# Performance work log

Hardware: AMD Instinct MI355X
Metric: run time of the kernel (lower is better)

## Reference

```python
import jax, jax.numpy as jnp
import numpy as np

V, E, H, O = 25000, 300, 512, 1
B, T = 128, 512


def setup_inputs() -> dict:
    key = jax.random.key(0)
    ks = jax.random.split(key, 8)
    # xavier-uniform style init for weight matrices
    def xav(k, shape):
        fan_in, fan_out = shape[1], shape[0]
        lim = jnp.sqrt(6.0 / (fan_in + fan_out)).astype(jnp.float32)
        return jax.random.uniform(k, shape, jnp.float32, -lim, lim)
    x = jax.random.randint(ks[0], (B, T), 0, V)
    h0 = jnp.zeros((1, B, H), jnp.float32)
    c0 = jnp.zeros((1, B, H), jnp.float32)
    emb = jax.random.normal(ks[1], (V, E), jnp.float32)
    W_ih = xav(ks[2], (4 * H, E))
    W_hh = xav(ks[3], (4 * H, H))
    b_ih = jnp.zeros((4 * H,), jnp.float32)
    b_hh = jnp.zeros((4 * H,), jnp.float32)
    fc_w = xav(ks[4], (O, H))
    fc_b = jnp.zeros((O,), jnp.float32)
    return {"x": x, "h0": h0, "c0": c0, "emb": emb, "W_ih": W_ih,
            "W_hh": W_hh, "b_ih": b_ih, "b_hh": b_hh, "fc_w": fc_w, "fc_b": fc_b}


def reference(x, h0, c0, emb, W_ih, W_hh, b_ih, b_hh, fc_w, fc_b):
    # embedding lookup: [B, T, E]
    embed = emb[x]
    # precompute input projections for all timesteps: [T, B, 4H]
    gates_x = jnp.einsum('bte,ge->tbg', embed, W_ih) + b_ih + b_hh

    def step(carry, gx):
        h, c = carry  # [B, H], [B, H]
        gates = gx + h @ W_hh.T  # [B, 4H]
        i, f, g, o = jnp.split(gates, 4, axis=-1)
        i = jax.nn.sigmoid(i)
        f = jax.nn.sigmoid(f)
        g = jnp.tanh(g)
        o = jax.nn.sigmoid(o)
        c = f * c + i * g
        h = o * jnp.tanh(c)
        return (h, c), h

    (h_T, c_T), hs = jax.lax.scan(step, (h0[0], c0[0]), gates_x)
    output = jnp.transpose(hs, (1, 0, 2))[None]  # [1, B, T, H]
    h_out = output[:, :, -1:]                     # [1, B, 1, H]
    c_out = c_T[None]                             # [1, B, H]
    y = h_out @ fc_w.T + fc_b                     # [1, B, 1, O]
    return y, h_out, c_out
```

## Files before the change

kernel.cpp:

```cpp
#include <hip/hip_runtime.h>

#define VOCAB 25000
#define EDIM  300
#define EPAD  320
#define HDIM  512
#define BATCH 128
#define TLEN  512
#define NTHR  512

typedef __attribute__((ext_vector_type(8))) short short8;
typedef __attribute__((ext_vector_type(4))) float f32x4;
typedef unsigned int u32;
typedef unsigned long long u64;

static __device__ __forceinline__ unsigned short f2bf(float f) {
    unsigned int u = __float_as_uint(f);
    unsigned int r = u + 0x7fffu + ((u >> 16) & 1u);
    return (unsigned short)(r >> 16);
}

__global__ void conv_pad_row(const float* __restrict__ src, unsigned short* __restrict__ dst,
                             int rows, int cs, int cd) {
    for (int r = blockIdx.x; r < rows; r += gridDim.x)
        for (int c = threadIdx.x; c < cd; c += blockDim.x)
            dst[(long)r * cd + c] = (c < cs) ? f2bf(src[(long)r * cs + c]) : (unsigned short)0;
}

__global__ __launch_bounds__(NTHR, 2) void lstm_pers(
    const int* __restrict__ x, const float* __restrict__ h0, const float* __restrict__ c0,
    const float* __restrict__ b_ih, const float* __restrict__ b_hh,
    const unsigned short* __restrict__ embb, const unsigned short* __restrict__ wihb,
    const unsigned short* __restrict__ whhb, u32* __restrict__ hb, float* __restrict__ out) {
    const int tid  = threadIdx.x;
    const int bt   = blockIdx.x & 7;
    const int jt   = blockIdx.x >> 3;
    const int m0   = bt * 16;
    const int lane = tid & 63;
    const int wv   = tid >> 6;
    const int gate = wv >> 1, jsub = wv & 1;
    const int g0   = gate * HDIM + jt * 32 + jsub * 16;
    const int r    = lane & 15;
    const int q    = lane >> 4;
    const int sw   = r & 7;

    const int bl = tid >> 5, jl = tid & 31;
    const int bg = m0 + bl, jg = jt * 32 + jl;

    __shared__ alignas(16) unsigned short h_lds[16 * 512];
    __shared__ alignas(16) unsigned short emb_lds[2][16 * 320];
    __shared__ int x_lds[16 * TLEN];
    __shared__ float lds_g[4][16][36];

    const int brow = g0 + r;
    const unsigned short* whp = whhb + (long)brow * HDIM + q * 8;
    const unsigned short* wip = wihb + (long)brow * EPAD + q * 8;
#define LDH(i) short8 wh##i = *(const short8*)(whp + i * 32);
#define LDE(i) short8 wi##i = *(const short8*)(wip + i * 32);
    LDH(0) LDH(1) LDH(2) LDH(3) LDH(4) LDH(5) LDH(6) LDH(7)
    LDH(8) LDH(9) LDH(10) LDH(11) LDH(12) LDH(13) LDH(14) LDH(15)
    LDE(0) LDE(1) LDE(2) LDE(3) LDE(4) LDE(5) LDE(6) LDE(7) LDE(8) LDE(9)
#undef LDH
#undef LDE

    for (int i = tid; i < 16 * TLEN; i += NTHR)
        x_lds[i] = x[(m0 + (i >> 9)) * TLEN + (i & 511)];

    const float bsum0 = b_ih[0 * HDIM + jg] + b_hh[0 * HDIM + jg];
    const float bsum1 = b_ih[1 * HDIM + jg] + b_hh[1 * HDIM + jg];
    const float bsum2 = b_ih[2 * HDIM + jg] + b_hh[2 * HDIM + jg];
    const float bsum3 = b_ih[3 * HDIM + jg] + b_hh[3 * HDIM + jg];

    float c_reg = c0[bg * HDIM + jg];
    float h_reg = h0[bg * HDIM + jg];

    u32* const hb0 = hb;
    u32* const hb1 = hb + BATCH * HDIM;
    __hip_atomic_store(hb0 + bg * HDIM + jg, (u32)f2bf(h_reg),
                       __ATOMIC_RELAXED, __HIP_MEMORY_SCOPE_AGENT);

    u32 hoff[8], lofs[8];
#pragma unroll
    for (int k = 0; k < 8; ++k) {
        int u   = tid + k * NTHR;
        int row = u >> 8, col = u & 255;
        hoff[k] = (u32)((m0 + row) * 256 + col);
        int chunk = col >> 2, sub = col & 3;
        lofs[k] = (u32)(row * 512 + ((chunk ^ (row & 7)) * 4 + sub) * 2);
    }

    __syncthreads();
    {
        int row = tid / 40, cc = tid - row * 40;
        int tok = x_lds[row * TLEN];
        *(short8*)&emb_lds[0][row * 320 + ((cc ^ (row & 7)) * 8)] =
            *(const short8*)(embb + (long)tok * EPAD + cc * 8);
        if (tid < 128) {
            int i1 = tid + NTHR; int row2 = i1 / 40, cc2 = i1 - row2 * 40;
            int tok2 = x_lds[row2 * TLEN];
            *(short8*)&emb_lds[0][row2 * 320 + ((cc2 ^ (row2 & 7)) * 8)] =
                *(const short8*)(embb + (long)tok2 * EPAD + cc2 * 8);
        }
    }
    __syncthreads();

    for (int t = 0; t < TLEN; ++t) {
        const int pb = t & 1;
        const u64* hsrc = (const u64*)(pb ? hb1 : hb0);
        u64 hv[8];
#pragma unroll
        for (int k = 0; k < 8; ++k)
            hv[k] = __hip_atomic_load(hsrc + hoff[k], __ATOMIC_RELAXED, __HIP_MEMORY_SCOPE_AGENT);

        {
            int tn = (t + 1 < TLEN) ? (t + 1) : (TLEN - 1);
            unsigned short* ebuf = (unsigned short*)emb_lds[pb ^ 1];
            int row = tid / 40, cc = tid - row * 40;
            int tok = x_lds[row * TLEN + tn];
            *(short8*)&ebuf[row * 320 + ((cc ^ (row & 7)) * 8)] =
                *(const short8*)(embb + (long)tok * EPAD + cc * 8);
            if (tid < 128) {
                int i1 = tid + NTHR; int row2 = i1 / 40, cc2 = i1 - row2 * 40;
                int tok2 = x_lds[row2 * TLEN + tn];
                *(short8*)&ebuf[row2 * 320 + ((cc2 ^ (row2 & 7)) * 8)] =
                    *(const short8*)(embb + (long)tok2 * EPAD + cc2 * 8);
            }
        }

        const unsigned short* ecur = (const unsigned short*)emb_lds[pb];
        f32x4 ae = {0.f, 0.f, 0.f, 0.f};
        short8 a;
#define ME(i) a = *(const short8*)&ecur[r * 320 + (((q + 4 * i) ^ sw) * 8)]; \
              ae = __builtin_amdgcn_mfma_f32_16x16x32_bf16(a, wi##i, ae, 0, 0, 0);
        ME(0) ME(1) ME(2) ME(3) ME(4) ME(5) ME(6) ME(7) ME(8) ME(9)
#undef ME

        const u32 want = (u32)t;
        while (1) {
            u32 bad = 0;
#pragma unroll
            for (int k = 0; k < 8; ++k)
                bad |= (((u32)(hv[k] >> 16) & 0xFFFFu) ^ want) | (((u32)(hv[k] >> 48)) ^ want);
            if (!bad) break;
#pragma unroll
            for (int k = 0; k < 8; ++k)
                hv[k] = __hip_atomic_load(hsrc + hoff[k], __ATOMIC_RELAXED, __HIP_MEMORY_SCOPE_AGENT);
        }

#pragma unroll
        for (int k = 0; k < 8; ++k) {
            u32 two = ((u32)hv[k] & 0xFFFFu) | (((u32)(hv[k] >> 32) & 0xFFFFu) << 16);
            *(u32*)&h_lds[lofs[k]] = two;
        }
        __syncthreads();

        f32x4 ah = {0.f, 0.f, 0.f, 0.f};
#define MH(i) a = *(const short8*)&h_lds[r * 512 + (((q + 4 * i) ^ sw) * 8)]; \
              ah = __builtin_amdgcn_mfma_f32_16x16x32_bf16(a, wh##i, ah, 0, 0, 0);
        MH(0) MH(1) MH(2) MH(3) MH(4) MH(5) MH(6) MH(7)
        MH(8) MH(9) MH(10) MH(11) MH(12) MH(13) MH(14) MH(15)
#undef MH

        const int crow = q * 4;
        const int ccol = jsub * 16 + r;
#pragma unroll
        for (int rr = 0; rr < 4; ++rr) lds_g[gate][crow + rr][ccol] = ah[rr] + ae[rr];
        __syncthreads();

        float gi = lds_g[0][bl][jl] + bsum0;
        float gf = lds_g[1][bl][jl] + bsum1;
        float gg = lds_g[2][bl][jl] + bsum2;
        float go = lds_g[3][bl][jl] + bsum3;
        float si = 1.f / (1.f + __expf(-gi));
        float sf = 1.f / (1.f + __expf(-gf));
        float tg = 2.f / (1.f + __expf(-2.f * gg)) - 1.f;
        float so = 1.f / (1.f + __expf(-go));
        c_reg = sf * c_reg + si * tg;
        float th = 2.f / (1.f + __expf(-2.f * c_reg)) - 1.f;
        h_reg = so * th;
        u32* dst = (pb ? hb0 : hb1) + bg * HDIM + jg;
        __hip_atomic_store(dst, ((u32)(t + 1) << 16) | (u32)f2bf(h_reg),
                           __ATOMIC_RELAXED, __HIP_MEMORY_SCOPE_AGENT);
        __syncthreads();
    }

    out[BATCH + bg * HDIM + jg] = h_reg;
    out[BATCH + BATCH * HDIM + bg * HDIM + jg] = c_reg;
}

__global__ void fc_k(const float* __restrict__ h, const float* __restrict__ fcw,
                     const float* __restrict__ fcb, float* __restrict__ y) {
    int b = blockIdx.x * 4 + (threadIdx.x >> 6);
    int lane = threadIdx.x & 63;
    float s = 0.f;
#pragma unroll
    for (int j = lane; j < HDIM; j += 64) s += h[b * HDIM + j] * fcw[j];
#pragma unroll
    for (int off = 32; off; off >>= 1) s += __shfl_down(s, off, 64);
    if (lane == 0) y[b] = s + fcb[0];
}

extern "C" void kernel_launch(void* const* d_in, const int* in_sizes, int n_in,
                              void* d_out, int out_size, void* d_ws, size_t ws_size,
                              hipStream_t stream) {
    const int*   x   = (const int*)d_in[0];
    const float* h0  = (const float*)d_in[1];
    const float* c0  = (const float*)d_in[2];
    const float* emb = (const float*)d_in[3];
    const float* Wih = (const float*)d_in[4];
    const float* Whh = (const float*)d_in[5];
    const float* bih = (const float*)d_in[6];
    const float* bhh = (const float*)d_in[7];
    const float* fcw = (const float*)d_in[8];
    const float* fcb = (const float*)d_in[9];
    float* out = (float*)d_out;

    char* ws = (char*)d_ws;
    unsigned short* embb = (unsigned short*)(ws);
    unsigned short* wihb = (unsigned short*)(ws + 16000000);
    unsigned short* whhb = (unsigned short*)(ws + 17310720);
    u32*            hb   = (u32*)(ws + 19407872);

    conv_pad_row<<<4096, 256, 0, stream>>>(emb, embb, VOCAB, EDIM, EPAD);
    conv_pad_row<<<2048, 256, 0, stream>>>(Wih, wihb, 4 * HDIM, EDIM, EPAD);
    conv_pad_row<<<2048, 256, 0, stream>>>(Whh, whhb, 4 * HDIM, HDIM, HDIM);

    void* args[] = {(void*)&x, (void*)&h0, (void*)&c0, (void*)&bih, (void*)&bhh,
                    (void*)&embb, (void*)&wihb, (void*)&whhb, (void*)&hb, (void*)&out};
    hipLaunchCooperativeKernel((void*)lstm_pers, dim3(128), dim3(NTHR), args, 0, stream);

    fc_k<<<32, 256, 0, stream>>>(out + BATCH, fcw, fcb, out);
}
```

Before: 1.607 ms.

## Split MFMA accumulator chains, defer embedding LDS stores, use LDS-only barriers

The per-step MFMA reductions now use several independent accumulators (two for the input projection, four for the recurrent one), which breaks the serial dependency chain between back-to-back MFMAs. The next-step embedding gather is loaded into registers early and written to LDS only after the recurrent MFMAs, so the global load latency is hidden behind the spin-wait and compute. __syncthreads is replaced by a barrier that waits only on LDS counters, so outstanding global atomics and loads are not drained at each barrier. This relies on the atomic h store needing no vmcnt wait before the barrier, and the extra accumulators cost registers.

```diff
diff --git a/kernel.cpp b/kernel.cpp
--- a/kernel.cpp
+++ b/kernel.cpp
@@ -12,6 +12,13 @@
 typedef __attribute__((ext_vector_type(4))) float f32x4;
 typedef unsigned int u32;
 typedef unsigned long long u64;
+
+#define BAR_LDS() do {                                        \
+    asm volatile("s_waitcnt lgkmcnt(0)" ::: "memory");        \
+    __builtin_amdgcn_sched_barrier(0);                        \
+    __builtin_amdgcn_s_barrier();                             \
+    __builtin_amdgcn_sched_barrier(0);                        \
+} while (0)
 
 static __device__ __forceinline__ unsigned short f2bf(float f) {
     unsigned int u = __float_as_uint(f);
@@ -88,17 +95,19 @@
         lofs[k] = (u32)(row * 512 + ((chunk ^ (row & 7)) * 4 + sub) * 2);
     }
 
+    const int row0 = tid / 40,            cc0 = tid - row0 * 40;
+    const int i1   = NTHR + (tid & 127);
+    const int row1 = i1 / 40,             cc1 = i1 - row1 * 40;
+
     __syncthreads();
     {
-        int row = tid / 40, cc = tid - row * 40;
-        int tok = x_lds[row * TLEN];
-        *(short8*)&emb_lds[0][row * 320 + ((cc ^ (row & 7)) * 8)] =
-            *(const short8*)(embb + (long)tok * EPAD + cc * 8);
+        int tok0 = x_lds[row0 * TLEN];
+        *(short8*)&emb_lds[0][row0 * 320 + ((cc0 ^ (row0 & 7)) * 8)] =
+            *(const short8*)(embb + (long)tok0 * EPAD + cc0 * 8);
         if (tid < 128) {
-            int i1 = tid + NTHR; int row2 = i1 / 40, cc2 = i1 - row2 * 40;
-            int tok2 = x_lds[row2 * TLEN];
-            *(short8*)&emb_lds[0][row2 * 320 + ((cc2 ^ (row2 & 7)) * 8)] =
-                *(const short8*)(embb + (long)tok2 * EPAD + cc2 * 8);
+            int tok1 = x_lds[row1 * TLEN];
+            *(short8*)&emb_lds[0][row1 * 320 + ((cc1 ^ (row1 & 7)) * 8)] =
+                *(const short8*)(embb + (long)tok1 * EPAD + cc1 * 8);
         }
     }
     __syncthreads();
@@ -111,28 +120,22 @@
         for (int k = 0; k < 8; ++k)
             hv[k] = __hip_atomic_load(hsrc + hoff[k], __ATOMIC_RELAXED, __HIP_MEMORY_SCOPE_AGENT);
 
+        const int tn = (t + 1 < TLEN) ? (t + 1) : (TLEN - 1);
+        short8 ev0 = *(const short8*)(embb + (long)x_lds[row0 * TLEN + tn] * EPAD + cc0 * 8);
+        short8 ev1 = *(const short8*)(embb + (long)x_lds[row1 * TLEN + tn] * EPAD + cc1 * 8);
+        __builtin_amdgcn_sched_barrier(0);
+
+        const unsigned short* ecur = (const unsigned short*)emb_lds[pb];
+        f32x4 ae0 = {0.f, 0.f, 0.f, 0.f}, ae1 = {0.f, 0.f, 0.f, 0.f};
         {
-            int tn = (t + 1 < TLEN) ? (t + 1) : (TLEN - 1);
-            unsigned short* ebuf = (unsigned short*)emb_lds[pb ^ 1];
-            int row = tid / 40, cc = tid - row * 40;
-            int tok = x_lds[row * TLEN + tn];
-            *(short8*)&ebuf[row * 320 + ((cc ^ (row & 7)) * 8)] =
-                *(const short8*)(embb + (long)tok * EPAD + cc * 8);
-            if (tid < 128) {
-                int i1 = tid + NTHR; int row2 = i1 / 40, cc2 = i1 - row2 * 40;
-                int tok2 = x_lds[row2 * TLEN + tn];
-                *(short8*)&ebuf[row2 * 320 + ((cc2 ^ (row2 & 7)) * 8)] =
-                    *(const short8*)(embb + (long)tok2 * EPAD + cc2 * 8);
-            }
-        }
-
-        const unsigned short* ecur = (const unsigned short*)emb_lds[pb];
-        f32x4 ae = {0.f, 0.f, 0.f, 0.f};
-        short8 a;
-#define ME(i) a = *(const short8*)&ecur[r * 320 + (((q + 4 * i) ^ sw) * 8)]; \
-              ae = __builtin_amdgcn_mfma_f32_16x16x32_bf16(a, wi##i, ae, 0, 0, 0);
-        ME(0) ME(1) ME(2) ME(3) ME(4) ME(5) ME(6) ME(7) ME(8) ME(9)
+            short8 a;
+#define ME(i, A) a = *(const short8*)&ecur[r * 320 + (((q + 4 * i) ^ sw) * 8)]; \
+                 A = __builtin_amdgcn_mfma_f32_16x16x32_bf16(a, wi##i, A, 0, 0, 0);
+            ME(0, ae0) ME(1, ae1) ME(2, ae0) ME(3, ae1) ME(4, ae0)
+            ME(5, ae1) ME(6, ae0) ME(7, ae1) ME(8, ae0) ME(9, ae1)
 #undef ME
+        }
+        __builtin_amdgcn_sched_barrier(0);
 
         const u32 want = (u32)t;
         while (1) {
@@ -151,20 +154,35 @@
             u32 two = ((u32)hv[k] & 0xFFFFu) | (((u32)(hv[k] >> 32) & 0xFFFFu) << 16);
             *(u32*)&h_lds[lofs[k]] = two;
         }
-        __syncthreads();
-
-        f32x4 ah = {0.f, 0.f, 0.f, 0.f};
-#define MH(i) a = *(const short8*)&h_lds[r * 512 + (((q + 4 * i) ^ sw) * 8)]; \
-              ah = __builtin_amdgcn_mfma_f32_16x16x32_bf16(a, wh##i, ah, 0, 0, 0);
-        MH(0) MH(1) MH(2) MH(3) MH(4) MH(5) MH(6) MH(7)
-        MH(8) MH(9) MH(10) MH(11) MH(12) MH(13) MH(14) MH(15)
+        BAR_LDS();
+
+        f32x4 ah0 = {0.f, 0.f, 0.f, 0.f}, ah1 = {0.f, 0.f, 0.f, 0.f};
+        f32x4 ah2 = {0.f, 0.f, 0.f, 0.f}, ah3 = {0.f, 0.f, 0.f, 0.f};
+        {
+            short8 a;
+#define MH(i, A) a = *(const short8*)&h_lds[r * 512 + (((q + 4 * i) ^ sw) * 8)]; \
+                 A = __builtin_amdgcn_mfma_f32_16x16x32_bf16(a, wh##i, A, 0, 0, 0);
+            MH(0, ah0) MH(1, ah1) MH(2, ah2) MH(3, ah3)
+            MH(4, ah0) MH(5, ah1) MH(6, ah2) MH(7, ah3)
+            MH(8, ah0) MH(9, ah1) MH(10, ah2) MH(11, ah3)
+            MH(12, ah0) MH(13, ah1) MH(14, ah2) MH(15, ah3)
 #undef MH
-
+        }
+        __builtin_amdgcn_sched_barrier(0);
+
+        {
+            unsigned short* ebuf = (unsigned short*)emb_lds[pb ^ 1];
+            *(short8*)&ebuf[row0 * 320 + ((cc0 ^ (row0 & 7)) * 8)] = ev0;
+            if (tid < 128)
+                *(short8*)&ebuf[row1 * 320 + ((cc1 ^ (row1 & 7)) * 8)] = ev1;
+        }
+
+        f32x4 s = (ah0 + ah1) + (ah2 + ah3) + (ae0 + ae1);
         const int crow = q * 4;
         const int ccol = jsub * 16 + r;
 #pragma unroll
-        for (int rr = 0; rr < 4; ++rr) lds_g[gate][crow + rr][ccol] = ah[rr] + ae[rr];
-        __syncthreads();
+        for (int rr = 0; rr < 4; ++rr) lds_g[gate][crow + rr][ccol] = s[rr];
+        BAR_LDS();
 
         float gi = lds_g[0][bl][jl] + bsum0;
         float gf = lds_g[1][bl][jl] + bsum1;
@@ -180,7 +198,7 @@
         u32* dst = (pb ? hb0 : hb1) + bg * HDIM + jg;
         __hip_atomic_store(dst, ((u32)(t + 1) << 16) | (u32)f2bf(h_reg),
                            __ATOMIC_RELAXED, __HIP_MEMORY_SCOPE_AGENT);
-        __syncthreads();
+        BAR_LDS();
     }
 
     out[BATCH + bg * HDIM + jg] = h_reg;
```

New measurement: 1.495 ms. 1.07x faster.
